# Kernel tuning notes

Hardware: AMD Instinct MI355X
Metric: run time of the kernel (lower is better)

Reference implementation:

```python
import jax, jax.numpy as jnp
import numpy as np

N_NODES = 50000
N_EDGES = 600000
D_FEAT = 128
HIDDEN = 128
N_CLASSES = 47


def setup_inputs() -> dict:
    key = jax.random.key(0)
    ks = jax.random.split(key, 8)
    x = jax.random.normal(ks[0], (N_NODES, D_FEAT), dtype=jnp.float32)
    edge_index = jax.random.randint(ks[1], (2, N_EDGES), 0, N_NODES, dtype=jnp.int64)
    def glorot(k, shape):
        fan_in, fan_out = shape
        s = jnp.sqrt(2.0 / (fan_in + fan_out)).astype(jnp.float32)
        return jax.random.normal(k, shape, dtype=jnp.float32) * s
    return {
        "x": x,
        "edge_index": edge_index,
        "Wl0": glorot(ks[2], (D_FEAT, HIDDEN)),
        "bl0": jnp.zeros((HIDDEN,), jnp.float32),
        "Wr0": glorot(ks[3], (D_FEAT, HIDDEN)),
        "Wl1": glorot(ks[4], (HIDDEN, HIDDEN)),
        "bl1": jnp.zeros((HIDDEN,), jnp.float32),
        "Wr1": glorot(ks[5], (HIDDEN, HIDDEN)),
        "Wl2": glorot(ks[6], (HIDDEN, N_CLASSES)),
        "bl2": jnp.zeros((N_CLASSES,), jnp.float32),
        "Wr2": glorot(ks[7], (HIDDEN, N_CLASSES)),
    }


def _sage_conv(x, src, dst, Wl, bl, Wr, n_nodes):
    # mean-aggregate neighbor (source) features at destination nodes
    msg = x[src]                                                  # [E, D] gather
    agg = jax.ops.segment_sum(msg, dst, num_segments=n_nodes)     # [N, D]
    deg = jax.ops.segment_sum(jnp.ones((src.shape[0],), x.dtype), dst,
                              num_segments=n_nodes)               # [N]
    agg = agg / jnp.maximum(deg, 1.0)[:, None]
    # PyG SAGEConv: lin_l(aggr) + lin_r(x_root); bias lives in lin_l
    return agg @ Wl + bl + x @ Wr


def reference(x, edge_index, Wl0, bl0, Wr0, Wl1, bl1, Wr1, Wl2, bl2, Wr2):
    src, dst = edge_index[0], edge_index[1]
    n = x.shape[0]
    h = jax.nn.relu(_sage_conv(x, src, dst, Wl0, bl0, Wr0, n))
    h = jax.nn.relu(_sage_conv(h, src, dst, Wl1, bl1, Wr1, n))
    h = _sage_conv(h, src, dst, Wl2, bl2, Wr2, n)
    # F.normalize(p=2, dim=-1): eps-clamped L2 norm (torch eps=1e-12)
    norm = jnp.maximum(jnp.linalg.norm(h, axis=-1, keepdims=True), 1e-12)
    h = h / norm
    return jax.nn.log_softmax(h, axis=1)
```

## Files before the change

### kernel.cpp

```cpp
#include <hip/hip_runtime.h>
#include <stdint.h>

#define N_NODES 50000
#define N_EDGES 600000
#define NCLS    47
#define SCAN_TPB 512
#define SCAN_BLOCKS ((N_NODES + SCAN_TPB - 1) / SCAN_TPB)

typedef __attribute__((ext_vector_type(8))) short short8;
typedef __attribute__((ext_vector_type(4))) float f32x4;

static __device__ __forceinline__ float bf2f(uint16_t h) {
    union { uint32_t u; float f; } c; c.u = ((uint32_t)h) << 16; return c.f;
}
static __device__ __forceinline__ float bf2fs(short h) { return bf2f((uint16_t)h); }
static __device__ __forceinline__ uint16_t f2bf(float f) {
    union { float f; uint32_t u; } c; c.f = f;
    uint32_t u = c.u;
    return (uint16_t)((u + 0x7fffu + ((u >> 16) & 1u)) >> 16);
}

__global__ __launch_bounds__(256) void k_split(const float4* __restrict__ x,
                                               ushort4* __restrict__ xh,
                                               ushort4* __restrict__ xl) {
    int i = blockIdx.x * 256 + threadIdx.x;
    float4 v = x[i];
    ushort4 h, l;
    h.x = f2bf(v.x); l.x = f2bf(v.x - bf2f(h.x));
    h.y = f2bf(v.y); l.y = f2bf(v.y - bf2f(h.y));
    h.z = f2bf(v.z); l.z = f2bf(v.z - bf2f(h.z));
    h.w = f2bf(v.w); l.w = f2bf(v.w - bf2f(h.w));
    xh[i] = h;
    xl[i] = l;
}

__global__ __launch_bounds__(256) void k_cvt_idx(const int* __restrict__ ei,
                                                 int* __restrict__ src,
                                                 int* __restrict__ dst,
                                                 int* __restrict__ deg) {
    __shared__ int is64;
    {
        int lane = threadIdx.x;
        if (lane < 64) {
            int f = ei[2 * lane + 1] | ei[2 * lane + 129];
            unsigned long long m = __ballot(f != 0);
            if (lane == 0) is64 = (m == 0ULL) ? 1 : 0;
        }
        __syncthreads();
    }
    int e = blockIdx.x * 256 + threadIdx.x;
    if (e < N_EDGES) {
        int s, d;
        if (is64) { s = ei[2 * e]; d = ei[2 * (N_EDGES + e)]; }
        else      { s = ei[e];     d = ei[N_EDGES + e]; }
        s = min(max(s, 0), N_NODES - 1);
        d = min(max(d, 0), N_NODES - 1);
        src[e] = s;
        dst[e] = d;
        atomicAdd(&deg[d], 1);
    }
}

__global__ __launch_bounds__(SCAN_TPB) void k_scan1(const int* __restrict__ deg,
                                                    int* __restrict__ partial) {
    int t = blockIdx.x * SCAN_TPB + threadIdx.x;
    int v = (t < N_NODES) ? deg[t] : 0;
#pragma unroll
    for (int o = 1; o < 64; o <<= 1) v += __shfl_xor(v, o);
    __shared__ int ws[SCAN_TPB / 64];
    int lane = threadIdx.x & 63, w = threadIdx.x >> 6;
    if (lane == 0) ws[w] = v;
    __syncthreads();
    if (threadIdx.x == 0) {
        int s = 0;
#pragma unroll
        for (int i = 0; i < SCAN_TPB / 64; ++i) s += ws[i];
        partial[blockIdx.x] = s;
    }
}

__global__ __launch_bounds__(128) void k_scan2(int* __restrict__ partial) {
    __shared__ int sh[128];
    int t = threadIdx.x;
    int v = (t < SCAN_BLOCKS) ? partial[t] : 0;
    sh[t] = v;
    __syncthreads();
    for (int o = 1; o < 128; o <<= 1) {
        int u = (t >= o) ? sh[t - o] : 0;
        __syncthreads();
        sh[t] += u;
        __syncthreads();
    }
    if (t < SCAN_BLOCKS) partial[t] = sh[t] - v;
}

__global__ __launch_bounds__(SCAN_TPB) void k_scan3(const int* __restrict__ deg,
                                                    const int* __restrict__ partial,
                                                    int* __restrict__ row_start,
                                                    int* __restrict__ fill,
                                                    float* __restrict__ inv_deg) {
    int tb = threadIdx.x;
    int t = blockIdx.x * SCAN_TPB + tb;
    int v = (t < N_NODES) ? deg[t] : 0;
    int lane = tb & 63, w = tb >> 6;
    int inc = v;
#pragma unroll
    for (int o = 1; o < 64; o <<= 1) {
        int u = __shfl_up(inc, o);
        if (lane >= o) inc += u;
    }
    __shared__ int wsum[SCAN_TPB / 64];
    if (lane == 63) wsum[w] = inc;
    __syncthreads();
    int woff = 0;
    for (int i = 0; i < w; ++i) woff += wsum[i];
    int excl = partial[blockIdx.x] + woff + (inc - v);
    if (t < N_NODES) {
        row_start[t] = excl;
        fill[t] = excl;
        inv_deg[t] = 1.0f / (float)(v > 0 ? v : 1);
    }
}

__global__ __launch_bounds__(256) void k_fill(const int* __restrict__ src,
                                              const int* __restrict__ dst,
                                              int* __restrict__ fill,
                                              int* __restrict__ elist) {
    int e = blockIdx.x * 256 + threadIdx.x;
    if (e < N_EDGES) {
        int pos = atomicAdd(&fill[dst[e]], 1);
        elist[pos] = src[e];
    }
}

__global__ __launch_bounds__(256) void k_agg(const uint16_t* __restrict__ hm_h,
                                             const int* __restrict__ row_start,
                                             const int* __restrict__ degv,
                                             const float* __restrict__ inv_deg,
                                             const int* __restrict__ elist,
                                             uint16_t* __restrict__ agg_h,
                                             uint16_t* __restrict__ agg_l) {
    int lane = threadIdx.x & 63;
    int node = blockIdx.x * 4 + (threadIdx.x >> 6);
    if (node >= N_NODES) return;
    int g = lane >> 4;
    int li = lane & 15;
    int j = li * 8;
    int rs = row_start[node];
    int d = degv[node];
    float a[8];
#pragma unroll
    for (int k = 0; k < 8; ++k) a[k] = 0.f;
    int i = g;
    for (; i + 4 < d; i += 8) {
        int s0 = elist[rs + i];
        int s1 = elist[rs + i + 4];
        short8 w0 = *(const short8*)&hm_h[(size_t)s0 * 128 + j];
        short8 w1 = *(const short8*)&hm_h[(size_t)s1 * 128 + j];
#pragma unroll
        for (int k = 0; k < 8; ++k) a[k] += bf2fs(w0[k]) + bf2fs(w1[k]);
    }
    if (i < d) {
        int s = elist[rs + i];
        short8 w = *(const short8*)&hm_h[(size_t)s * 128 + j];
#pragma unroll
        for (int k = 0; k < 8; ++k) a[k] += bf2fs(w[k]);
    }
    float sc = inv_deg[node];
    short8 oh, ol;
#pragma unroll
    for (int k = 0; k < 8; ++k) {
        float v = a[k];
        v += __shfl_xor(v, 16);
        v += __shfl_xor(v, 32);
        v *= sc;
        uint16_t h = f2bf(v);
        oh[k] = (short)h;
        ol[k] = (short)f2bf(v - bf2f(h));
    }
    if (g == 0)      *(short8*)&agg_h[(size_t)node * 128 + j] = oh;
    else if (g == 1) *(short8*)&agg_l[(size_t)node * 128 + j] = ol;
}

__global__ __launch_bounds__(256) void k_prepw(const float* Wl0, const float* Wr0,
                                               const float* Wl1, const float* Wr1,
                                               const float* Wl2, const float* Wr2,
                                               uint16_t* __restrict__ img) {
    int b = blockIdx.x >> 6;
    int sub = blockIdx.x & 63;
    const float* W; int ncol, npad; uint16_t* o;
    switch (b) {
        case 0: W = Wl0; ncol = 128; npad = 128; o = img;           break;
        case 1: W = Wr0; ncol = 128; npad = 128; o = img + 32768;   break;
        case 2: W = Wl1; ncol = 128; npad = 128; o = img + 65536;   break;
        case 3: W = Wr1; ncol = 128; npad = 128; o = img + 98304;   break;
        case 4: W = Wl2; ncol = 47;  npad = 48;  o = img + 131072;  break;
        default:W = Wr2; ncol = 47;  npad = 48;  o = img + 143360;  break;
    }
    int elems = npad * 128;
    int i = sub * 256 + threadIdx.x;
    if (i < elems) {
        int col = i % npad, k = i / npad;
        float v = (col < ncol) ? W[k * ncol + col] : 0.f;
        uint16_t h = f2bf(v);
        uint16_t l = f2bf(v - bf2f(h));
        int idx;
        if (b < 4) idx = col * 128 + (((k >> 3) ^ (col & 15)) << 3) + (k & 7);
        else       idx = col * 128 + k;
        o[idx] = h;
        o[idx + elems] = l;
    }
}

__global__ __launch_bounds__(512) void k_gemm(const uint16_t* __restrict__ A1h,
                                              const uint16_t* __restrict__ A1l,
                                              const uint16_t* __restrict__ A2h,
                                              const uint16_t* __restrict__ A2l,
                                              const uint16_t* __restrict__ wl,
                                              const uint16_t* __restrict__ wr,
                                              const float* __restrict__ bias,
                                              uint16_t* __restrict__ outh,
                                              uint16_t* __restrict__ outl) {
    __shared__ __align__(16) uint16_t ldsW[32768];
    int tid = threadIdx.x;
    int lane = tid & 63, wv = tid >> 6;
    int li = lane & 15, g4 = lane >> 4;
    int mrow = blockIdx.x * 128 + wv * 16 + li;
    int r0 = min(mrow, N_NODES - 1);

    f32x4 acc[8];
#pragma unroll
    for (int t = 0; t < 8; ++t) acc[t] = (f32x4){0.f, 0.f, 0.f, 0.f};

#pragma unroll
    for (int arr = 0; arr < 2; ++arr) {
        {
            const uint4* g = (const uint4*)(arr ? wr : wl);
            uint4* l = (uint4*)ldsW;
#pragma unroll
            for (int j2 = 0; j2 < 8; ++j2)
                l[j2 * 512 + tid] = g[j2 * 512 + tid];
        }
        __syncthreads();

        const uint16_t* Ah = arr ? A2h : A1h;
        const uint16_t* Al = arr ? A2l : A1l;
#pragma unroll
        for (int s = 0; s < 4; ++s) {
            int ko = s * 32 + g4 * 8;
            short8 a0h = *(const short8*)&Ah[(size_t)r0 * 128 + ko];
            short8 a0l = *(const short8*)&Al[(size_t)r0 * 128 + ko];
#pragma unroll
            for (int t = 0; t < 8; ++t) {
                int off = (t * 16 + li) * 128 + (((s * 4 + g4) ^ li) << 3);
                short8 bh = *(const short8*)&ldsW[off];
                short8 bl = *(const short8*)&ldsW[off + 16384];
                acc[t] = __builtin_amdgcn_mfma_f32_16x16x32_bf16(a0h, bh, acc[t], 0, 0, 0);
                acc[t] = __builtin_amdgcn_mfma_f32_16x16x32_bf16(a0l, bh, acc[t], 0, 0, 0);
                acc[t] = __builtin_amdgcn_mfma_f32_16x16x32_bf16(a0h, bl, acc[t], 0, 0, 0);
            }
        }
        if (arr == 0) __syncthreads();
    }
    int rowbase = blockIdx.x * 128 + wv * 16 + g4 * 4;
#pragma unroll
    for (int t = 0; t < 8; ++t) {
        int col = t * 16 + li;
        float bv = bias[col];
#pragma unroll
        for (int rr = 0; rr < 4; ++rr) {
            int row = rowbase + rr;
            if (row < N_NODES) {
                float v = fmaxf(acc[t][rr] + bv, 0.f);
                uint16_t h = f2bf(v);
                outh[(size_t)row * 128 + col] = h;
                outl[(size_t)row * 128 + col] = f2bf(v - bf2f(h));
            }
        }
    }
}

__global__ __launch_bounds__(256) void k_gemm2(const uint16_t* __restrict__ A1h,
                                               const uint16_t* __restrict__ A1l,
                                               const uint16_t* __restrict__ A2h,
                                               const uint16_t* __restrict__ A2l,
                                               const uint16_t* __restrict__ wl,
                                               const uint16_t* __restrict__ wr,
                                               const float* __restrict__ bias,
                                               float* __restrict__ out) {
    int tid = threadIdx.x;
    int lane = tid & 63, wv = tid >> 6;
    int li = lane & 15, g4 = lane >> 4;
    int mrow = blockIdx.x * 64 + wv * 16 + li;
    int r = min(mrow, N_NODES - 1);

    f32x4 acc[3];
#pragma unroll
    for (int t = 0; t < 3; ++t) acc[t] = (f32x4){0.f, 0.f, 0.f, 0.f};

#pragma unroll
    for (int arr = 0; arr < 2; ++arr) {
        const uint16_t* Ah = arr ? A2h : A1h;
        const uint16_t* Al = arr ? A2l : A1l;
        const uint16_t* W  = arr ? wr : wl;
#pragma unroll
        for (int s = 0; s < 4; ++s) {
            int ko = s * 32 + g4 * 8;
            short8 ah = *(const short8*)&Ah[(size_t)r * 128 + ko];
            short8 al = *(const short8*)&Al[(size_t)r * 128 + ko];
#pragma unroll
            for (int t = 0; t < 3; ++t) {
                const uint16_t* p = &W[(t * 16 + li) * 128 + ko];
                short8 bh = *(const short8*)p;
                short8 bl = *(const short8*)(p + 6144);
                acc[t] = __builtin_amdgcn_mfma_f32_16x16x32_bf16(ah, bh, acc[t], 0, 0, 0);
                acc[t] = __builtin_amdgcn_mfma_f32_16x16x32_bf16(al, bh, acc[t], 0, 0, 0);
                acc[t] = __builtin_amdgcn_mfma_f32_16x16x32_bf16(ah, bl, acc[t], 0, 0, 0);
            }
        }
    }

    float b0 = bias[li];
    float b1 = bias[16 + li];
    bool v2ok = (li < 15);
    float b2 = v2ok ? bias[32 + li] : 0.f;

    int rowbase = blockIdx.x * 64 + wv * 16 + g4 * 4;
#pragma unroll
    for (int rr = 0; rr < 4; ++rr) {
        int row = rowbase + rr;
        float v0 = acc[0][rr] + b0;
        float v1 = acc[1][rr] + b1;
        float v2 = v2ok ? (acc[2][rr] + b2) : 0.f;
        float ss = v0 * v0 + v1 * v1 + v2 * v2;
        ss += __shfl_xor(ss, 1);
        ss += __shfl_xor(ss, 2);
        ss += __shfl_xor(ss, 4);
        ss += __shfl_xor(ss, 8);
        float inv = 1.f / fmaxf(sqrtf(ss), 1e-12f);
        v0 *= inv; v1 *= inv; v2 *= inv;
        float mx = fmaxf(v0, v1);
        if (v2ok) mx = fmaxf(mx, v2);
        mx = fmaxf(mx, __shfl_xor(mx, 1));
        mx = fmaxf(mx, __shfl_xor(mx, 2));
        mx = fmaxf(mx, __shfl_xor(mx, 4));
        mx = fmaxf(mx, __shfl_xor(mx, 8));
        float se = expf(v0 - mx) + expf(v1 - mx) + (v2ok ? expf(v2 - mx) : 0.f);
        se += __shfl_xor(se, 1);
        se += __shfl_xor(se, 2);
        se += __shfl_xor(se, 4);
        se += __shfl_xor(se, 8);
        float lse = logf(se);
        if (row < N_NODES) {
            size_t ob = (size_t)row * NCLS;
            out[ob + li]      = v0 - mx - lse;
            out[ob + 16 + li] = v1 - mx - lse;
            if (v2ok) out[ob + 32 + li] = v2 - mx - lse;
        }
    }
}

extern "C" void kernel_launch(void* const* d_in, const int* in_sizes, int n_in,
                              void* d_out, int out_size, void* d_ws, size_t ws_size,
                              hipStream_t stream) {
    const float* x   = (const float*)d_in[0];
    const int*   ei  = (const int*)d_in[1];
    const float* Wl0 = (const float*)d_in[2];
    const float* bl0 = (const float*)d_in[3];
    const float* Wr0 = (const float*)d_in[4];
    const float* Wl1 = (const float*)d_in[5];
    const float* bl1 = (const float*)d_in[6];
    const float* Wr1 = (const float*)d_in[7];
    const float* Wl2 = (const float*)d_in[8];
    const float* bl2 = (const float*)d_in[9];
    const float* Wr2 = (const float*)d_in[10];
    float* out = (float*)d_out;

    char* ws = (char*)d_ws;
    size_t cur = 0;
    auto alloc = [&](size_t bytes) {
        char* p = ws + cur;
        cur += (bytes + 255) & ~(size_t)255;
        return p;
    };
    const size_t MATB = (size_t)N_NODES * 128 * 2;
    int*      deg       = (int*)alloc(N_NODES * 4);
    int*      row_start = (int*)alloc(N_NODES * 4);
    int*      fill      = (int*)alloc(N_NODES * 4);
    float*    inv_deg   = (float*)alloc(N_NODES * 4);
    int*      partial   = (int*)alloc(SCAN_BLOCKS * 4);
    int*      src       = (int*)alloc(N_EDGES * 4);
    int*      dst       = (int*)alloc(N_EDGES * 4);
    int*      elist     = (int*)alloc(N_EDGES * 4);
    uint16_t* wimg      = (uint16_t*)alloc(155648 * 2);
    uint16_t* xh        = (uint16_t*)alloc(MATB);
    uint16_t* xl        = (uint16_t*)alloc(MATB);
    uint16_t* Ah        = (uint16_t*)alloc(MATB);
    uint16_t* Al        = (uint16_t*)alloc(MATB);
    uint16_t* Bh        = (uint16_t*)alloc(MATB);
    uint16_t* Bl        = (uint16_t*)alloc(MATB);
    uint16_t* Ch        = (uint16_t*)alloc(MATB);
    uint16_t* Cl        = (uint16_t*)alloc(MATB);

    hipMemsetAsync(deg, 0, N_NODES * 4, stream);
    k_prepw<<<384, 256, 0, stream>>>(Wl0, Wr0, Wl1, Wr1, Wl2, Wr2, wimg);
    k_split<<<(N_NODES * 128 / 4) / 256, 256, 0, stream>>>((const float4*)x,
                                                           (ushort4*)xh, (ushort4*)xl);

    int egrid = (N_EDGES + 255) / 256;
    k_cvt_idx<<<egrid, 256, 0, stream>>>(ei, src, dst, deg);
    k_scan1<<<SCAN_BLOCKS, SCAN_TPB, 0, stream>>>(deg, partial);
    k_scan2<<<1, 128, 0, stream>>>(partial);
    k_scan3<<<SCAN_BLOCKS, SCAN_TPB, 0, stream>>>(deg, partial, row_start, fill, inv_deg);
    k_fill<<<egrid, 256, 0, stream>>>(src, dst, fill, elist);

    int agrid = (N_NODES + 3) / 4;
    int ggrid = (N_NODES + 127) / 128;
    int g2grid = (N_NODES + 63) / 64;

    k_agg<<<agrid, 256, 0, stream>>>(xh, row_start, deg, inv_deg, elist, Ah, Al);
    k_gemm<<<ggrid, 512, 0, stream>>>(Ah, Al, xh, xl, wimg, wimg + 32768, bl0, Bh, Bl);
    k_agg<<<agrid, 256, 0, stream>>>(Bh, row_start, deg, inv_deg, elist, Ah, Al);
    k_gemm<<<ggrid, 512, 0, stream>>>(Ah, Al, Bh, Bl, wimg + 65536, wimg + 98304, bl1, Ch, Cl);
    k_agg<<<agrid, 256, 0, stream>>>(Ch, row_start, deg, inv_deg, elist, Ah, Al);
    k_gemm2<<<g2grid, 256, 0, stream>>>(Ah, Al, Ch, Cl, wimg + 131072, wimg + 143360, bl2, out);
}
```

Measured before the change: 324.4 us.

## Drop low-half activation splits, fuse index conversion, stage final weights in LDS

Activations are now stored only as a single bf16 tensor. The low-order residual arrays and their MFMA passes are removed from the split, aggregate and both GEMM kernels, which cuts memory traffic and matrix work; the weights keep their hi/lo split. The src/dst conversion buffers are eliminated: degree counting reads the raw edge_index, and fill decodes it again directly. The final GEMM now loads the swizzled classifier weights into LDS and uses 512-thread blocks covering 128 rows. The trade-off is reduced precision in intermediate activations.

```diff
diff --git a/kernel.cpp b/kernel.cpp
--- a/kernel.cpp
+++ b/kernel.cpp
@@ -21,23 +21,19 @@
 }
 
 __global__ __launch_bounds__(256) void k_split(const float4* __restrict__ x,
-                                               ushort4* __restrict__ xh,
-                                               ushort4* __restrict__ xl) {
+                                               ushort4* __restrict__ xh) {
     int i = blockIdx.x * 256 + threadIdx.x;
     float4 v = x[i];
-    ushort4 h, l;
-    h.x = f2bf(v.x); l.x = f2bf(v.x - bf2f(h.x));
-    h.y = f2bf(v.y); l.y = f2bf(v.y - bf2f(h.y));
-    h.z = f2bf(v.z); l.z = f2bf(v.z - bf2f(h.z));
-    h.w = f2bf(v.w); l.w = f2bf(v.w - bf2f(h.w));
+    ushort4 h;
+    h.x = f2bf(v.x);
+    h.y = f2bf(v.y);
+    h.z = f2bf(v.z);
+    h.w = f2bf(v.w);
     xh[i] = h;
-    xl[i] = l;
-}
-
-__global__ __launch_bounds__(256) void k_cvt_idx(const int* __restrict__ ei,
-                                                 int* __restrict__ src,
-                                                 int* __restrict__ dst,
-                                                 int* __restrict__ deg) {
+}
+
+__global__ __launch_bounds__(256) void k_deg(const int* __restrict__ ei,
+                                             int* __restrict__ deg) {
     __shared__ int is64;
     {
         int lane = threadIdx.x;
@@ -50,13 +46,8 @@
     }
     int e = blockIdx.x * 256 + threadIdx.x;
     if (e < N_EDGES) {
-        int s, d;
-        if (is64) { s = ei[2 * e]; d = ei[2 * (N_EDGES + e)]; }
-        else      { s = ei[e];     d = ei[N_EDGES + e]; }
-        s = min(max(s, 0), N_NODES - 1);
+        int d = is64 ? ei[2 * (N_EDGES + e)] : ei[N_EDGES + e];
         d = min(max(d, 0), N_NODES - 1);
-        src[e] = s;
-        dst[e] = d;
         atomicAdd(&deg[d], 1);
     }
 }
@@ -122,14 +113,28 @@
     }
 }
 
-__global__ __launch_bounds__(256) void k_fill(const int* __restrict__ src,
-                                              const int* __restrict__ dst,
+__global__ __launch_bounds__(256) void k_fill(const int* __restrict__ ei,
                                               int* __restrict__ fill,
                                               int* __restrict__ elist) {
+    __shared__ int is64;
+    {
+        int lane = threadIdx.x;
+        if (lane < 64) {
+            int f = ei[2 * lane + 1] | ei[2 * lane + 129];
+            unsigned long long m = __ballot(f != 0);
+            if (lane == 0) is64 = (m == 0ULL) ? 1 : 0;
+        }
+        __syncthreads();
+    }
     int e = blockIdx.x * 256 + threadIdx.x;
     if (e < N_EDGES) {
-        int pos = atomicAdd(&fill[dst[e]], 1);
-        elist[pos] = src[e];
+        int s, d;
+        if (is64) { s = ei[2 * e]; d = ei[2 * (N_EDGES + e)]; }
+        else      { s = ei[e];     d = ei[N_EDGES + e]; }
+        s = min(max(s, 0), N_NODES - 1);
+        d = min(max(d, 0), N_NODES - 1);
+        int pos = atomicAdd(&fill[d], 1);
+        elist[pos] = s;
     }
 }
 
@@ -138,8 +143,7 @@
                                              const int* __restrict__ degv,
                                              const float* __restrict__ inv_deg,
                                              const int* __restrict__ elist,
-                                             uint16_t* __restrict__ agg_h,
-                                             uint16_t* __restrict__ agg_l) {
+                                             uint16_t* __restrict__ agg_h) {
     int lane = threadIdx.x & 63;
     int node = blockIdx.x * 4 + (threadIdx.x >> 6);
     if (node >= N_NODES) return;
@@ -167,19 +171,15 @@
         for (int k = 0; k < 8; ++k) a[k] += bf2fs(w[k]);
     }
     float sc = inv_deg[node];
-    short8 oh, ol;
+    short8 oh;
 #pragma unroll
     for (int k = 0; k < 8; ++k) {
         float v = a[k];
         v += __shfl_xor(v, 16);
         v += __shfl_xor(v, 32);
-        v *= sc;
-        uint16_t h = f2bf(v);
-        oh[k] = (short)h;
-        ol[k] = (short)f2bf(v - bf2f(h));
-    }
-    if (g == 0)      *(short8*)&agg_h[(size_t)node * 128 + j] = oh;
-    else if (g == 1) *(short8*)&agg_l[(size_t)node * 128 + j] = ol;
+        oh[k] = (short)f2bf(v * sc);
+    }
+    if (g == 0) *(short8*)&agg_h[(size_t)node * 128 + j] = oh;
 }
 
 __global__ __launch_bounds__(256) void k_prepw(const float* Wl0, const float* Wr0,
@@ -204,23 +204,18 @@
         float v = (col < ncol) ? W[k * ncol + col] : 0.f;
         uint16_t h = f2bf(v);
         uint16_t l = f2bf(v - bf2f(h));
-        int idx;
-        if (b < 4) idx = col * 128 + (((k >> 3) ^ (col & 15)) << 3) + (k & 7);
-        else       idx = col * 128 + k;
+        int idx = col * 128 + (((k >> 3) ^ (col & 15)) << 3) + (k & 7);
         o[idx] = h;
         o[idx + elems] = l;
     }
 }
 
 __global__ __launch_bounds__(512) void k_gemm(const uint16_t* __restrict__ A1h,
-                                              const uint16_t* __restrict__ A1l,
                                               const uint16_t* __restrict__ A2h,
-                                              const uint16_t* __restrict__ A2l,
                                               const uint16_t* __restrict__ wl,
                                               const uint16_t* __restrict__ wr,
                                               const float* __restrict__ bias,
-                                              uint16_t* __restrict__ outh,
-                                              uint16_t* __restrict__ outl) {
+                                              uint16_t* __restrict__ outh) {
     __shared__ __align__(16) uint16_t ldsW[32768];
     int tid = threadIdx.x;
     int lane = tid & 63, wv = tid >> 6;
@@ -244,19 +239,16 @@
         __syncthreads();
 
         const uint16_t* Ah = arr ? A2h : A1h;
-        const uint16_t* Al = arr ? A2l : A1l;
 #pragma unroll
         for (int s = 0; s < 4; ++s) {
             int ko = s * 32 + g4 * 8;
             short8 a0h = *(const short8*)&Ah[(size_t)r0 * 128 + ko];
-            short8 a0l = *(const short8*)&Al[(size_t)r0 * 128 + ko];
 #pragma unroll
             for (int t = 0; t < 8; ++t) {
                 int off = (t * 16 + li) * 128 + (((s * 4 + g4) ^ li) << 3);
                 short8 bh = *(const short8*)&ldsW[off];
                 short8 bl = *(const short8*)&ldsW[off + 16384];
                 acc[t] = __builtin_amdgcn_mfma_f32_16x16x32_bf16(a0h, bh, acc[t], 0, 0, 0);
-                acc[t] = __builtin_amdgcn_mfma_f32_16x16x32_bf16(a0l, bh, acc[t], 0, 0, 0);
                 acc[t] = __builtin_amdgcn_mfma_f32_16x16x32_bf16(a0h, bl, acc[t], 0, 0, 0);
             }
         }
@@ -270,29 +262,32 @@
 #pragma unroll
         for (int rr = 0; rr < 4; ++rr) {
             int row = rowbase + rr;
-            if (row < N_NODES) {
-                float v = fmaxf(acc[t][rr] + bv, 0.f);
-                uint16_t h = f2bf(v);
-                outh[(size_t)row * 128 + col] = h;
-                outl[(size_t)row * 128 + col] = f2bf(v - bf2f(h));
-            }
-        }
-    }
-}
-
-__global__ __launch_bounds__(256) void k_gemm2(const uint16_t* __restrict__ A1h,
-                                               const uint16_t* __restrict__ A1l,
+            if (row < N_NODES)
+                outh[(size_t)row * 128 + col] = f2bf(fmaxf(acc[t][rr] + bv, 0.f));
+        }
+    }
+}
+
+__global__ __launch_bounds__(512) void k_gemm2(const uint16_t* __restrict__ A1h,
                                                const uint16_t* __restrict__ A2h,
-                                               const uint16_t* __restrict__ A2l,
-                                               const uint16_t* __restrict__ wl,
-                                               const uint16_t* __restrict__ wr,
+                                               const uint16_t* __restrict__ w2,
                                                const float* __restrict__ bias,
                                                float* __restrict__ out) {
+    __shared__ __align__(16) uint16_t ldsW[24576];
     int tid = threadIdx.x;
     int lane = tid & 63, wv = tid >> 6;
     int li = lane & 15, g4 = lane >> 4;
-    int mrow = blockIdx.x * 64 + wv * 16 + li;
+    int mrow = blockIdx.x * 128 + wv * 16 + li;
     int r = min(mrow, N_NODES - 1);
+
+    {
+        const uint4* g = (const uint4*)w2;
+        uint4* l = (uint4*)ldsW;
+#pragma unroll
+        for (int j2 = 0; j2 < 12; ++j2)
+            l[j2 * 512 + tid] = g[j2 * 512 + tid];
+    }
+    __syncthreads();
 
     f32x4 acc[3];
 #pragma unroll
@@ -301,20 +296,17 @@
 #pragma unroll
     for (int arr = 0; arr < 2; ++arr) {
         const uint16_t* Ah = arr ? A2h : A1h;
-        const uint16_t* Al = arr ? A2l : A1l;
-        const uint16_t* W  = arr ? wr : wl;
+        const uint16_t* WL = &ldsW[arr * 12288];
 #pragma unroll
         for (int s = 0; s < 4; ++s) {
             int ko = s * 32 + g4 * 8;
             short8 ah = *(const short8*)&Ah[(size_t)r * 128 + ko];
-            short8 al = *(const short8*)&Al[(size_t)r * 128 + ko];
 #pragma unroll
             for (int t = 0; t < 3; ++t) {
-                const uint16_t* p = &W[(t * 16 + li) * 128 + ko];
-                short8 bh = *(const short8*)p;
-                short8 bl = *(const short8*)(p + 6144);
+                int off = (t * 16 + li) * 128 + (((s * 4 + g4) ^ li) << 3);
+                short8 bh = *(const short8*)&WL[off];
+                short8 bl = *(const short8*)&WL[off + 6144];
                 acc[t] = __builtin_amdgcn_mfma_f32_16x16x32_bf16(ah, bh, acc[t], 0, 0, 0);
-                acc[t] = __builtin_amdgcn_mfma_f32_16x16x32_bf16(al, bh, acc[t], 0, 0, 0);
                 acc[t] = __builtin_amdgcn_mfma_f32_16x16x32_bf16(ah, bl, acc[t], 0, 0, 0);
             }
         }
@@ -325,7 +317,7 @@
     bool v2ok = (li < 15);
     float b2 = v2ok ? bias[32 + li] : 0.f;
 
-    int rowbase = blockIdx.x * 64 + wv * 16 + g4 * 4;
+    int rowbase = blockIdx.x * 128 + wv * 16 + g4 * 4;
 #pragma unroll
     for (int rr = 0; rr < 4; ++rr) {
         int row = rowbase + rr;
@@ -389,39 +381,31 @@
     int*      fill      = (int*)alloc(N_NODES * 4);
     float*    inv_deg   = (float*)alloc(N_NODES * 4);
     int*      partial   = (int*)alloc(SCAN_BLOCKS * 4);
-    int*      src       = (int*)alloc(N_EDGES * 4);
-    int*      dst       = (int*)alloc(N_EDGES * 4);
     int*      elist     = (int*)alloc(N_EDGES * 4);
     uint16_t* wimg      = (uint16_t*)alloc(155648 * 2);
     uint16_t* xh        = (uint16_t*)alloc(MATB);
-    uint16_t* xl        = (uint16_t*)alloc(MATB);
     uint16_t* Ah        = (uint16_t*)alloc(MATB);
-    uint16_t* Al        = (uint16_t*)alloc(MATB);
     uint16_t* Bh        = (uint16_t*)alloc(MATB);
-    uint16_t* Bl        = (uint16_t*)alloc(MATB);
     uint16_t* Ch        = (uint16_t*)alloc(MATB);
-    uint16_t* Cl        = (uint16_t*)alloc(MATB);
 
     hipMemsetAsync(deg, 0, N_NODES * 4, stream);
     k_prepw<<<384, 256, 0, stream>>>(Wl0, Wr0, Wl1, Wr1, Wl2, Wr2, wimg);
-    k_split<<<(N_NODES * 128 / 4) / 256, 256, 0, stream>>>((const float4*)x,
-                                                           (ushort4*)xh, (ushort4*)xl);
+    k_split<<<(N_NODES * 128 / 4) / 256, 256, 0, stream>>>((const float4*)x, (ushort4*)xh);
 
     int egrid = (N_EDGES + 255) / 256;
-    k_cvt_idx<<<egrid, 256, 0, stream>>>(ei, src, dst, deg);
+    k_deg<<<egrid, 256, 0, stream>>>(ei, deg);
     k_scan1<<<SCAN_BLOCKS, SCAN_TPB, 0, stream>>>(deg, partial);
     k_scan2<<<1, 128, 0, stream>>>(partial);
     k_scan3<<<SCAN_BLOCKS, SCAN_TPB, 0, stream>>>(deg, partial, row_start, fill, inv_deg);
-    k_fill<<<egrid, 256, 0, stream>>>(src, dst, fill, elist);
+    k_fill<<<egrid, 256, 0, stream>>>(ei, fill, elist);
 
     int agrid = (N_NODES + 3) / 4;
     int ggrid = (N_NODES + 127) / 128;
-    int g2grid = (N_NODES + 63) / 64;
-
-    k_agg<<<agrid, 256, 0, stream>>>(xh, row_start, deg, inv_deg, elist, Ah, Al);
-    k_gemm<<<ggrid, 512, 0, stream>>>(Ah, Al, xh, xl, wimg, wimg + 32768, bl0, Bh, Bl);
-    k_agg<<<agrid, 256, 0, stream>>>(Bh, row_start, deg, inv_deg, elist, Ah, Al);
-    k_gemm<<<ggrid, 512, 0, stream>>>(Ah, Al, Bh, Bl, wimg + 65536, wimg + 98304, bl1, Ch, Cl);
-    k_agg<<<agrid, 256, 0, stream>>>(Ch, row_start, deg, inv_deg, elist, Ah, Al);
-    k_gemm2<<<g2grid, 256, 0, stream>>>(Ah, Al, Ch, Cl, wimg + 131072, wimg + 143360, bl2, out);
-}
+
+    k_agg<<<agrid, 256, 0, stream>>>(xh, row_start, deg, inv_deg, elist, Ah);
+    k_gemm<<<ggrid, 512, 0, stream>>>(Ah, xh, wimg, wimg + 32768, bl0, Bh);
+    k_agg<<<agrid, 256, 0, stream>>>(Bh, row_start, deg, inv_deg, elist, Ah);
+    k_gemm<<<ggrid, 512, 0, stream>>>(Ah, Bh, wimg + 65536, wimg + 98304, bl1, Ch);
+    k_agg<<<agrid, 256, 0, stream>>>(Ch, row_start, deg, inv_deg, elist, Ah);
+    k_gemm2<<<ggrid, 512, 0, stream>>>(Ah, Ch, wimg + 131072, bl2, out);
+}
```

New measurement: 287.6 us. 11.3% less time.
